# Kernel optimization log

Measured on AMD Instinct MI355X. Metric: run time of the kernel, lower is better.

The kernel has to match this reference:

```python
import jax, jax.numpy as jnp
import numpy as np

B, N, D, H = 2, 2048, 1024, 8
DH = D // H  # head dim = 128


def setup_inputs() -> dict:
    key = jax.random.key(0)
    k0, k1, k2 = jax.random.split(key, 3)
    s = 1.0 / np.sqrt(D).astype(np.float32)
    return {
        "x": jax.random.normal(k0, (B, N, D), dtype=jnp.float32),
        "w_qkv": jax.random.normal(k1, (3 * D, D), dtype=jnp.float32) * s,
        "b_qkv": jnp.zeros((3 * D,), dtype=jnp.float32),
        "w_o": jax.random.normal(k2, (D, D), dtype=jnp.float32) * s,
        "b_o": jnp.zeros((D,), dtype=jnp.float32),
    }


def reference(x, w_qkv, b_qkv, w_o, b_o):
    b, n, d = x.shape
    h = H
    dh = d // h
    # qkv projection (torch Linear: x @ W.T + b)
    qkv = x @ w_qkv.T + b_qkv                      # [b, n, 3d]
    # rearrange 'b n (k d h) -> k b h n d': head index is INNERMOST
    qkv = qkv.reshape(b, n, 3, dh, h)              # [b, n, k, dh, h]
    qkv = jnp.transpose(qkv, (2, 0, 4, 1, 3))      # [k, b, h, n, dh]
    q, k, v = qkv[0], qkv[1], qkv[2]
    # unnormalized attention: NO softmax between the two einsums
    attn = jnp.einsum('bhik,bhjk->bhij', q, k)     # [b, h, n, n]
    out = jnp.einsum('bhik,bhkj->bhij', attn, v)   # [b, h, n, dh]
    # rearrange 'b h n d -> b n (h d)'
    out = jnp.transpose(out, (0, 2, 1, 3)).reshape(b, n, d)
    return out @ w_o.T + b_o
```

## Files before the change

### kernel.cpp

```cpp
#include <hip/hip_runtime.h>
#include <hip/hip_bf16.h>
#include <stdint.h>


typedef __bf16 bf16_t;
typedef __bf16 bf16x4 __attribute__((ext_vector_type(4)));
typedef __bf16 bf16x8 __attribute__((ext_vector_type(8)));
typedef float  fx4    __attribute__((ext_vector_type(4)));
typedef unsigned short u16;
typedef u16 u16x4 __attribute__((ext_vector_type(4)));
typedef u16 u16x8 __attribute__((ext_vector_type(8)));

typedef const void __attribute__((address_space(1)))* gas_ptr;
typedef void __attribute__((address_space(3)))*       las_ptr;

__device__ __forceinline__ void gl_lds16(const void* g, void* l) {
  __builtin_amdgcn_global_load_lds((gas_ptr)g, (las_ptr)l, 16, 0, 0);
}

#define SLAB 262144

__global__ __launch_bounds__(256) void beacon_kernel(float* out, float val, int n)
{
  const int i = blockIdx.x * 256 + threadIdx.x;
  if (i < n) out[i] = val;
}

__global__ __launch_bounds__(256) void conv_xw_kernel(
    const float* __restrict__ x, const float* __restrict__ wq,
    bf16_t* __restrict__ xb, bf16_t* __restrict__ wqkvb)
{
  const int i = blockIdx.x * 256 + threadIdx.x;
  const float* src; bf16_t* dst; int off;
  if (i < 1048576) { src = x;  dst = xb;    off = i; }
  else             { src = wq; dst = wqkvb; off = i - 1048576; }
  const float4 v = ((const float4*)src)[off];
  bf16x4 o;
  o[0] = (bf16_t)v.x; o[1] = (bf16_t)v.y; o[2] = (bf16_t)v.z; o[3] = (bf16_t)v.w;
  ((bf16x4*)dst)[off] = o;
}

__global__ __launch_bounds__(256) void conv_wo_kernel(
    const float* __restrict__ wo, bf16_t* __restrict__ wob)
{
  const int i = blockIdx.x * 256 + threadIdx.x;
  const float4 v = ((const float4*)wo)[i];
  bf16x4 o;
  o[0] = (bf16_t)v.x; o[1] = (bf16_t)v.y; o[2] = (bf16_t)v.z; o[3] = (bf16_t)v.w;
  ((bf16x4*)wob)[i] = o;
}

__global__ __launch_bounds__(256) void mfma_gemm_kernel(
    const bf16_t* __restrict__ A, const bf16_t* __restrict__ Bt,
    const float* __restrict__ bias, bf16_t* __restrict__ outb,
    float* __restrict__ outf, int ldc, int mode)
{
  __shared__ __align__(16) short As[128*32];
  __shared__ __align__(16) short Bs[128*32];
  const int t    = threadIdx.x;
  const int lane = t & 63;
  const int w    = t >> 6;
  const int wr   = (w >> 1) << 6;
  const int wc   = (w & 1) << 6;
  const int lrow = lane & 15;
  const int kq   = (lane >> 4) << 3;
  const int row0 = blockIdx.y * 128;
  const int col0 = blockIdx.x * 128;

  const int i0 = t, i1 = t + 256;
  const bf16_t* a0 = A  + (size_t)(row0 + (i0 >> 2)) * 1024 + ((i0 & 3) << 3);
  const bf16_t* a1 = A  + (size_t)(row0 + (i1 >> 2)) * 1024 + ((i1 & 3) << 3);
  const bf16_t* b0 = Bt + (size_t)(col0 + (i0 >> 2)) * 1024 + ((i0 & 3) << 3);
  const bf16_t* b1 = Bt + (size_t)(col0 + (i1 >> 2)) * 1024 + ((i1 & 3) << 3);
  short* sa0 = &As[i0 * 8]; short* sa1 = &As[i1 * 8];
  short* sb0 = &Bs[i0 * 8]; short* sb1 = &Bs[i1 * 8];

  fx4 acc[4][4] = {};

  for (int k0 = 0; k0 < 1024; k0 += 32) {
    gl_lds16(a0 + k0, sa0);
    gl_lds16(a1 + k0, sa1);
    gl_lds16(b0 + k0, sb0);
    gl_lds16(b1 + k0, sb1);
    __syncthreads();
    bf16x8 af[4], bfr[4];
#pragma unroll
    for (int i = 0; i < 4; ++i)
      af[i] = *(const bf16x8*)&As[(wr + i*16 + lrow)*32 + kq];
#pragma unroll
    for (int j = 0; j < 4; ++j)
      bfr[j] = *(const bf16x8*)&Bs[(wc + j*16 + lrow)*32 + kq];
#pragma unroll
    for (int i = 0; i < 4; ++i)
#pragma unroll
      for (int j = 0; j < 4; ++j)
        acc[i][j] = __builtin_amdgcn_mfma_f32_16x16x32_bf16(af[i], bfr[j], acc[i][j], 0, 0, 0);
    __syncthreads();
  }

#pragma unroll
  for (int j = 0; j < 4; ++j) {
    const int col = col0 + wc + j*16 + lrow;
    const float bv = bias[col];
#pragma unroll
    for (int i = 0; i < 4; ++i) {
#pragma unroll
      for (int r = 0; r < 4; ++r) {
        const int row = row0 + wr + i*16 + ((lane >> 4) << 2) + r;
        const float v = acc[i][j][r] + bv;
        if (mode == 0) outb[(size_t)row * ldc + col] = (bf16_t)v;
        else           outf[(size_t)row * ldc + col] = v;
      }
    }
  }
}

__global__ __launch_bounds__(256) void deint_kernel(
    const bf16_t* __restrict__ qkv, bf16_t* __restrict__ Qb,
    bf16_t* __restrict__ Kb, bf16_t* __restrict__ Vb)
{
  __shared__ u16 L[8][16][132];
  const int t    = threadIdx.x;
  const int kk   = blockIdx.x;
  const int tile = blockIdx.y;
  const int gr0  = tile * 16;
  const u16* src_base = (const u16*)qkv + (size_t)gr0 * 3072 + kk * 1024;

#pragma unroll
  for (int p = 0; p < 2; ++p) {
    const int task = t + p * 256;
    const int r = task >> 5, g = task & 31;
    const u16x8* s = (const u16x8*)(src_base + (size_t)r * 3072 + 32 * g);
    const u16x8 u0 = s[0], u1 = s[1], u2 = s[2], u3 = s[3];
#pragma unroll
    for (int hh = 0; hh < 8; ++hh) {
      u16x4 wv = { u0[hh], u1[hh], u2[hh], u3[hh] };
      *(u16x4*)&L[hh][r][4 * g] = wv;
    }
  }
  __syncthreads();

  const int b  = gr0 >> 11;
  const int n0 = gr0 & 2047;
  bf16_t* base = (kk == 0) ? Qb : (kk == 1 ? Kb : Vb);
#pragma unroll
  for (int p = 0; p < 8; ++p) {
    const int task = t + p * 256;
    const int hh = task >> 8, rem = task & 255;
    const int r = rem >> 4, q = rem & 15;
    const u16x4 w0 = *(const u16x4*)&L[hh][r][8 * q];
    const u16x4 w1 = *(const u16x4*)&L[hh][r][8 * q + 4];
    u16x8 wv = { w0[0], w0[1], w0[2], w0[3], w1[0], w1[1], w1[2], w1[3] };
    *(u16x8*)(base + (size_t)(b * 8 + hh) * SLAB + (size_t)(n0 + r) * 128 + 8 * q) = wv;
  }
}

__global__ __launch_bounds__(256) void kv_part(
    const bf16_t* __restrict__ Kb, const bf16_t* __restrict__ Vb,
    float* __restrict__ Mpart)
{
  __shared__ float Ksf[64][128];
  __shared__ float Vsf[64][64];
  const int t = threadIdx.x;
  const int ch = blockIdx.x >> 1, dh = blockIdx.x & 1, bh = blockIdx.y;
  const bf16_t* Kg = Kb + (size_t)bh * SLAB;
  const bf16_t* Vg = Vb + (size_t)bh * SLAB + dh * 64;
  const int e0 = (t >> 4) * 8, d0 = (t & 15) * 4;
  float acc[8][4] = {};

  for (int sub = 0; sub < 2; ++sub) {
    const int n0 = ch * 128 + sub * 64;
#pragma unroll
    for (int p = 0; p < 4; ++p) {
      const int idx = t + p * 256;
      const int r = idx >> 4, c = (idx & 15) * 8;
      const bf16x8 k8 = *(const bf16x8*)(Kg + (size_t)(n0 + r) * 128 + c);
      float4 f0 = { (float)k8[0], (float)k8[1], (float)k8[2], (float)k8[3] };
      float4 f1 = { (float)k8[4], (float)k8[5], (float)k8[6], (float)k8[7] };
      *(float4*)&Ksf[r][c]     = f0;
      *(float4*)&Ksf[r][c + 4] = f1;
    }
#pragma unroll
    for (int p = 0; p < 2; ++p) {
      const int idx = t + p * 256;
      const int r = idx >> 3, c = (idx & 7) * 8;
      const bf16x8 v8 = *(const bf16x8*)(Vg + (size_t)(n0 + r) * 128 + c);
      float4 f0 = { (float)v8[0], (float)v8[1], (float)v8[2], (float)v8[3] };
      float4 f1 = { (float)v8[4], (float)v8[5], (float)v8[6], (float)v8[7] };
      *(float4*)&Vsf[r][c]     = f0;
      *(float4*)&Vsf[r][c + 4] = f1;
    }
    __syncthreads();
    for (int n = 0; n < 64; ++n) {
      const float4 ka = *(const float4*)&Ksf[n][e0];
      const float4 kb = *(const float4*)&Ksf[n][e0 + 4];
      const float4 vv = *(const float4*)&Vsf[n][d0];
      const float kf[8] = { ka.x, ka.y, ka.z, ka.w, kb.x, kb.y, kb.z, kb.w };
      const float vf[4] = { vv.x, vv.y, vv.z, vv.w };
#pragma unroll
      for (int i = 0; i < 8; ++i)
#pragma unroll
        for (int j = 0; j < 4; ++j) acc[i][j] += kf[i] * vf[j];
    }
    __syncthreads();
  }

  float* op = Mpart + ((size_t)(bh * 16 + ch) << 14) + dh * 64;
#pragma unroll
  for (int i = 0; i < 8; ++i)
    *(float4*)&op[(e0 + i) * 128 + d0] = *(const float4*)&acc[i][0];
}

__global__ __launch_bounds__(256) void reduce_mt(
    const float* __restrict__ Mpart, bf16_t* __restrict__ Mt)
{
  const int t = threadIdx.x, bh = blockIdx.y;
  const int task = blockIdx.x * 256 + t;
  const int eo = task >> 7, d = task & 127;
  const float* base = Mpart + ((size_t)(bh * 16) << 14) + d;
  float s[8] = {};
#pragma unroll
  for (int ch = 0; ch < 16; ++ch) {
    const float* p = base + ((size_t)ch << 14) + (eo * 8) * 128;
#pragma unroll
    for (int j = 0; j < 8; ++j) s[j] += p[j * 128];
  }
  u16x8 wv;
#pragma unroll
  for (int j = 0; j < 8; ++j) { bf16_t b = (bf16_t)s[j]; wv[j] = *(u16*)&b; }
  *(u16x8*)(Mt + (size_t)bh * 16384 + (size_t)d * 128 + eo * 8) = wv;
}

__global__ __launch_bounds__(256) void qm_mfma_kernel(
    const bf16_t* __restrict__ Qb, const bf16_t* __restrict__ Mt,
    bf16_t* __restrict__ O)
{
  __shared__ __align__(16) short As[128*32];
  __shared__ __align__(16) short Bs[128*32];
  const int t    = threadIdx.x;
  const int lane = t & 63;
  const int w    = t >> 6;
  const int wr   = (w >> 1) << 6;
  const int wc   = (w & 1) << 6;
  const int lrow = lane & 15;
  const int kq   = (lane >> 4) << 3;
  const int row0 = blockIdx.x * 128;
  const int bh   = blockIdx.y;
  const bf16_t* A  = Qb + (size_t)bh * SLAB;
  const bf16_t* Bt = Mt + (size_t)bh * 16384;

  const int i0 = t, i1 = t + 256;
  const bf16_t* a0 = A  + (size_t)(row0 + (i0 >> 2)) * 128 + ((i0 & 3) << 3);
  const bf16_t* a1 = A  + (size_t)(row0 + (i1 >> 2)) * 128 + ((i1 & 3) << 3);
  const bf16_t* b0 = Bt + (size_t)(i0 >> 2) * 128 + ((i0 & 3) << 3);
  const bf16_t* b1 = Bt + (size_t)(i1 >> 2) * 128 + ((i1 & 3) << 3);
  short* sa0 = &As[i0 * 8]; short* sa1 = &As[i1 * 8];
  short* sb0 = &Bs[i0 * 8]; short* sb1 = &Bs[i1 * 8];

  fx4 acc[4][4] = {};

  for (int k0 = 0; k0 < 128; k0 += 32) {
    gl_lds16(a0 + k0, sa0);
    gl_lds16(a1 + k0, sa1);
    gl_lds16(b0 + k0, sb0);
    gl_lds16(b1 + k0, sb1);
    __syncthreads();
    bf16x8 af[4], bfr[4];
#pragma unroll
    for (int i = 0; i < 4; ++i)
      af[i] = *(const bf16x8*)&As[(wr + i*16 + lrow)*32 + kq];
#pragma unroll
    for (int j = 0; j < 4; ++j)
      bfr[j] = *(const bf16x8*)&Bs[(wc + j*16 + lrow)*32 + kq];
#pragma unroll
    for (int i = 0; i < 4; ++i)
#pragma unroll
      for (int j = 0; j < 4; ++j)
        acc[i][j] = __builtin_amdgcn_mfma_f32_16x16x32_bf16(af[i], bfr[j], acc[i][j], 0, 0, 0);
    __syncthreads();
  }

  const int b = bh >> 3, h = bh & 7;
  bf16_t* obase = O + (size_t)(b * 2048) * 1024 + h * 128;
#pragma unroll
  for (int j = 0; j < 4; ++j) {
    const int col = wc + j*16 + lrow;
#pragma unroll
    for (int i = 0; i < 4; ++i) {
#pragma unroll
      for (int r = 0; r < 4; ++r) {
        const int row = row0 + wr + i*16 + ((lane >> 4) << 2) + r;
        obase[(size_t)row * 1024 + col] = (bf16_t)acc[i][j][r];
      }
    }
  }
}

extern "C" void kernel_launch(void* const* d_in, const int* in_sizes, int n_in,
                              void* d_out, int out_size, void* d_ws, size_t ws_size,
                              hipStream_t stream) {
  float* out = (float*)d_out;
  dim3 blk(256);

  int ix = -1, iwq = -1, ibq = -1, iwo = -1, ibo = -1;
  if (n_in == 5) {
    for (int i = 0; i < 5; ++i) {
      switch (in_sizes[i]) {
        case 4194304: ix  = i; break;
        case 3145728: iwq = i; break;
        case 3072:    ibq = i; break;
        case 1048576: iwo = i; break;
        case 1024:    ibo = i; break;
        default: break;
      }
    }
  }
  if (ix < 0 || iwq < 0 || ibq < 0 || iwo < 0 || ibo < 0) {
    beacon_kernel<<<dim3((out_size + 255) / 256), blk, 0, stream>>>(out, 50000.0f, out_size);
    return;
  }
  const size_t NEEDED = (size_t)40 * 1048576;
  if (ws_size < NEEDED) {
    beacon_kernel<<<dim3((out_size + 255) / 256), blk, 0, stream>>>(out, 30000.0f, out_size);
    return;
  }

  char* ws = (char*)d_ws;
  bf16_t* xb     = (bf16_t*)(ws);
  bf16_t* Qb     = (bf16_t*)(ws);
  bf16_t* wqkvb  = (bf16_t*)(ws + (size_t)8  * 1048576);
  bf16_t* O      = (bf16_t*)(ws + (size_t)8  * 1048576);
  bf16_t* qkv_rm = (bf16_t*)(ws + (size_t)16 * 1048576);
  float*  Mpart  = (float*) (ws + (size_t)16 * 1048576);
  bf16_t* Mt     = (bf16_t*)(ws + (size_t)32 * 1048576);
  bf16_t* wob    = (bf16_t*)(ws + (size_t)33 * 1048576);
  bf16_t* Kb     = (bf16_t*)d_out;
  bf16_t* Vb     = (bf16_t*)d_out + 16 * SLAB;

  const float* bq = (const float*)d_in[ibq];
  const float* bo = (const float*)d_in[ibo];

  conv_xw_kernel  <<<dim3(7168),    blk, 0, stream>>>((const float*)d_in[ix],
                                                      (const float*)d_in[iwq], xb, wqkvb);
  mfma_gemm_kernel<<<dim3(24, 32),  blk, 0, stream>>>(xb, wqkvb, bq, qkv_rm, out, 3072, 0);
  deint_kernel    <<<dim3(3, 256),  blk, 0, stream>>>(qkv_rm, Qb, Kb, Vb);
  conv_wo_kernel  <<<dim3(1024),    blk, 0, stream>>>((const float*)d_in[iwo], wob);
  kv_part         <<<dim3(32, 16),  blk, 0, stream>>>(Kb, Vb, Mpart);
  reduce_mt       <<<dim3(8, 16),   blk, 0, stream>>>(Mpart, Mt);
  qm_mfma_kernel  <<<dim3(16, 16),  blk, 0, stream>>>(Qb, Mt, O);
  mfma_gemm_kernel<<<dim3(8, 32),   blk, 0, stream>>>(O, wob, bo, qkv_rm, out, 1024, 1);
}
```

Measured before the change: 188.2 us.

## Fold K^T V into output projection weights and permute QKV weights to drop deinterleave

```diff
diff --git a/kernel.cpp b/kernel.cpp
--- a/kernel.cpp
+++ b/kernel.cpp
@@ -8,7 +8,6 @@
 typedef __bf16 bf16x8 __attribute__((ext_vector_type(8)));
 typedef float  fx4    __attribute__((ext_vector_type(4)));
 typedef unsigned short u16;
-typedef u16 u16x4 __attribute__((ext_vector_type(4)));
 typedef u16 u16x8 __attribute__((ext_vector_type(8)));
 
 typedef const void __attribute__((address_space(1)))* gas_ptr;
@@ -18,42 +17,57 @@
   __builtin_amdgcn_global_load_lds((gas_ptr)g, (las_ptr)l, 16, 0, 0);
 }
 
-#define SLAB 262144
-
 __global__ __launch_bounds__(256) void beacon_kernel(float* out, float val, int n)
 {
   const int i = blockIdx.x * 256 + threadIdx.x;
   if (i < n) out[i] = val;
 }
 
-__global__ __launch_bounds__(256) void conv_xw_kernel(
+__global__ __launch_bounds__(256) void conv_all_kernel(
     const float* __restrict__ x, const float* __restrict__ wq,
-    bf16_t* __restrict__ xb, bf16_t* __restrict__ wqkvb)
+    const float* __restrict__ wo, const float* __restrict__ bq,
+    bf16_t* __restrict__ xb, bf16_t* __restrict__ wqkvb,
+    bf16_t* __restrict__ wob, float* __restrict__ bqp)
 {
   const int i = blockIdx.x * 256 + threadIdx.x;
-  const float* src; bf16_t* dst; int off;
-  if (i < 1048576) { src = x;  dst = xb;    off = i; }
-  else             { src = wq; dst = wqkvb; off = i - 1048576; }
-  const float4 v = ((const float4*)src)[off];
-  bf16x4 o;
-  o[0] = (bf16_t)v.x; o[1] = (bf16_t)v.y; o[2] = (bf16_t)v.z; o[3] = (bf16_t)v.w;
-  ((bf16x4*)dst)[off] = o;
-}
-
-__global__ __launch_bounds__(256) void conv_wo_kernel(
-    const float* __restrict__ wo, bf16_t* __restrict__ wob)
-{
-  const int i = blockIdx.x * 256 + threadIdx.x;
-  const float4 v = ((const float4*)wo)[i];
-  bf16x4 o;
-  o[0] = (bf16_t)v.x; o[1] = (bf16_t)v.y; o[2] = (bf16_t)v.z; o[3] = (bf16_t)v.w;
-  ((bf16x4*)wob)[i] = o;
+  if (i < 2097152) {
+    const float* src; bf16_t* dst; int soff, doff;
+    if (i < 1048576) { src = x; dst = xb; soff = i; doff = i; }
+    else if (i < 1835008) {
+      const int j  = i - 1048576;
+      const int rp = j >> 8, g = j & 255;
+      const int kk = rp >> 10, rem = rp & 1023;
+      const int hh = rem >> 7,  dd = rem & 127;
+      const int r  = kk * 1024 + dd * 8 + hh;
+      src = wq; dst = wqkvb; soff = r * 256 + g; doff = j;
+    } else {
+      const int j = i - 1835008;
+      src = wo; dst = wob; soff = j; doff = j;
+    }
+    const float4 v = ((const float4*)src)[soff];
+    bf16x4 o;
+    o[0] = (bf16_t)v.x; o[1] = (bf16_t)v.y; o[2] = (bf16_t)v.z; o[3] = (bf16_t)v.w;
+    ((bf16x4*)dst)[doff] = o;
+  } else if (i < 2097920) {
+    const int j = i - 2097152;
+    float4 v;
+    float* pv = (float*)&v;
+#pragma unroll
+    for (int q = 0; q < 4; ++q) {
+      const int cp = j * 4 + q;
+      const int kk = cp >> 10, rem = cp & 1023;
+      const int hh = rem >> 7,  dd = rem & 127;
+      pv[q] = bq[kk * 1024 + dd * 8 + hh];
+    }
+    ((float4*)bqp)[j] = v;
+  }
 }
 
 __global__ __launch_bounds__(256) void mfma_gemm_kernel(
-    const bf16_t* __restrict__ A, const bf16_t* __restrict__ Bt,
-    const float* __restrict__ bias, bf16_t* __restrict__ outb,
-    float* __restrict__ outf, int ldc, int mode)
+    const bf16_t* __restrict__ A, int lda,
+    const bf16_t* __restrict__ Bt0, int ldb, size_t bt_bstride,
+    const float* __restrict__ bias,
+    bf16_t* __restrict__ outb, float* __restrict__ outf, int ldc, int mode)
 {
   __shared__ __align__(16) short As[128*32];
   __shared__ __align__(16) short Bs[128*32];
@@ -66,12 +80,13 @@
   const int kq   = (lane >> 4) << 3;
   const int row0 = blockIdx.y * 128;
   const int col0 = blockIdx.x * 128;
+  const bf16_t* Bt = Bt0 + (row0 >= 2048 ? bt_bstride : (size_t)0);
 
   const int i0 = t, i1 = t + 256;
-  const bf16_t* a0 = A  + (size_t)(row0 + (i0 >> 2)) * 1024 + ((i0 & 3) << 3);
-  const bf16_t* a1 = A  + (size_t)(row0 + (i1 >> 2)) * 1024 + ((i1 & 3) << 3);
-  const bf16_t* b0 = Bt + (size_t)(col0 + (i0 >> 2)) * 1024 + ((i0 & 3) << 3);
-  const bf16_t* b1 = Bt + (size_t)(col0 + (i1 >> 2)) * 1024 + ((i1 & 3) << 3);
+  const bf16_t* a0 = A  + (size_t)(row0 + (i0 >> 2)) * lda + ((i0 & 3) << 3);
+  const bf16_t* a1 = A  + (size_t)(row0 + (i1 >> 2)) * lda + ((i1 & 3) << 3);
+  const bf16_t* b0 = Bt + (size_t)(col0 + (i0 >> 2)) * ldb + ((i0 & 3) << 3);
+  const bf16_t* b1 = Bt + (size_t)(col0 + (i1 >> 2)) * ldb + ((i1 & 3) << 3);
   short* sa0 = &As[i0 * 8]; short* sa1 = &As[i1 * 8];
   short* sb0 = &Bs[i0 * 8]; short* sb1 = &Bs[i1 * 8];
 
@@ -115,56 +130,16 @@
   }
 }
 
-__global__ __launch_bounds__(256) void deint_kernel(
-    const bf16_t* __restrict__ qkv, bf16_t* __restrict__ Qb,
-    bf16_t* __restrict__ Kb, bf16_t* __restrict__ Vb)
-{
-  __shared__ u16 L[8][16][132];
-  const int t    = threadIdx.x;
-  const int kk   = blockIdx.x;
-  const int tile = blockIdx.y;
-  const int gr0  = tile * 16;
-  const u16* src_base = (const u16*)qkv + (size_t)gr0 * 3072 + kk * 1024;
-
-#pragma unroll
-  for (int p = 0; p < 2; ++p) {
-    const int task = t + p * 256;
-    const int r = task >> 5, g = task & 31;
-    const u16x8* s = (const u16x8*)(src_base + (size_t)r * 3072 + 32 * g);
-    const u16x8 u0 = s[0], u1 = s[1], u2 = s[2], u3 = s[3];
-#pragma unroll
-    for (int hh = 0; hh < 8; ++hh) {
-      u16x4 wv = { u0[hh], u1[hh], u2[hh], u3[hh] };
-      *(u16x4*)&L[hh][r][4 * g] = wv;
-    }
-  }
-  __syncthreads();
-
-  const int b  = gr0 >> 11;
-  const int n0 = gr0 & 2047;
-  bf16_t* base = (kk == 0) ? Qb : (kk == 1 ? Kb : Vb);
-#pragma unroll
-  for (int p = 0; p < 8; ++p) {
-    const int task = t + p * 256;
-    const int hh = task >> 8, rem = task & 255;
-    const int r = rem >> 4, q = rem & 15;
-    const u16x4 w0 = *(const u16x4*)&L[hh][r][8 * q];
-    const u16x4 w1 = *(const u16x4*)&L[hh][r][8 * q + 4];
-    u16x8 wv = { w0[0], w0[1], w0[2], w0[3], w1[0], w1[1], w1[2], w1[3] };
-    *(u16x8*)(base + (size_t)(b * 8 + hh) * SLAB + (size_t)(n0 + r) * 128 + 8 * q) = wv;
-  }
-}
-
 __global__ __launch_bounds__(256) void kv_part(
-    const bf16_t* __restrict__ Kb, const bf16_t* __restrict__ Vb,
-    float* __restrict__ Mpart)
+    const bf16_t* __restrict__ qkv, float* __restrict__ Mpart)
 {
   __shared__ float Ksf[64][128];
   __shared__ float Vsf[64][64];
   const int t = threadIdx.x;
   const int ch = blockIdx.x >> 1, dh = blockIdx.x & 1, bh = blockIdx.y;
-  const bf16_t* Kg = Kb + (size_t)bh * SLAB;
-  const bf16_t* Vg = Vb + (size_t)bh * SLAB + dh * 64;
+  const int b = bh >> 3, h = bh & 7;
+  const bf16_t* Kg = qkv + (size_t)(b * 2048) * 3072 + 1024 + h * 128;
+  const bf16_t* Vg = qkv + (size_t)(b * 2048) * 3072 + 2048 + h * 128 + dh * 64;
   const int e0 = (t >> 4) * 8, d0 = (t & 15) * 4;
   float acc[8][4] = {};
 
@@ -174,7 +149,7 @@
     for (int p = 0; p < 4; ++p) {
       const int idx = t + p * 256;
       const int r = idx >> 4, c = (idx & 15) * 8;
-      const bf16x8 k8 = *(const bf16x8*)(Kg + (size_t)(n0 + r) * 128 + c);
+      const bf16x8 k8 = *(const bf16x8*)(Kg + (size_t)(n0 + r) * 3072 + c);
       float4 f0 = { (float)k8[0], (float)k8[1], (float)k8[2], (float)k8[3] };
       float4 f1 = { (float)k8[4], (float)k8[5], (float)k8[6], (float)k8[7] };
       *(float4*)&Ksf[r][c]     = f0;
@@ -184,7 +159,7 @@
     for (int p = 0; p < 2; ++p) {
       const int idx = t + p * 256;
       const int r = idx >> 3, c = (idx & 7) * 8;
-      const bf16x8 v8 = *(const bf16x8*)(Vg + (size_t)(n0 + r) * 128 + c);
+      const bf16x8 v8 = *(const bf16x8*)(Vg + (size_t)(n0 + r) * 3072 + c);
       float4 f0 = { (float)v8[0], (float)v8[1], (float)v8[2], (float)v8[3] };
       float4 f1 = { (float)v8[4], (float)v8[5], (float)v8[6], (float)v8[7] };
       *(float4*)&Vsf[r][c]     = f0;
@@ -211,29 +186,31 @@
     *(float4*)&op[(e0 + i) * 128 + d0] = *(const float4*)&acc[i][0];
 }
 
-__global__ __launch_bounds__(256) void reduce_mt(
-    const float* __restrict__ Mpart, bf16_t* __restrict__ Mt)
+__global__ __launch_bounds__(256) void reduce_m(
+    const float* __restrict__ Mpart, bf16_t* __restrict__ Mb)
 {
   const int t = threadIdx.x, bh = blockIdx.y;
   const int task = blockIdx.x * 256 + t;
-  const int eo = task >> 7, d = task & 127;
-  const float* base = Mpart + ((size_t)(bh * 16) << 14) + d;
+  const int e = task >> 4, doct = task & 15;
+  const float* base = Mpart + ((size_t)(bh * 16) << 14) + e * 128 + doct * 8;
   float s[8] = {};
 #pragma unroll
   for (int ch = 0; ch < 16; ++ch) {
-    const float* p = base + ((size_t)ch << 14) + (eo * 8) * 128;
-#pragma unroll
-    for (int j = 0; j < 8; ++j) s[j] += p[j * 128];
+    const float* p = base + ((size_t)ch << 14);
+    const float4 v0 = *(const float4*)p;
+    const float4 v1 = *(const float4*)(p + 4);
+    s[0] += v0.x; s[1] += v0.y; s[2] += v0.z; s[3] += v0.w;
+    s[4] += v1.x; s[5] += v1.y; s[6] += v1.z; s[7] += v1.w;
   }
   u16x8 wv;
 #pragma unroll
-  for (int j = 0; j < 8; ++j) { bf16_t b = (bf16_t)s[j]; wv[j] = *(u16*)&b; }
-  *(u16x8*)(Mt + (size_t)bh * 16384 + (size_t)d * 128 + eo * 8) = wv;
-}
-
-__global__ __launch_bounds__(256) void qm_mfma_kernel(
-    const bf16_t* __restrict__ Qb, const bf16_t* __restrict__ Mt,
-    bf16_t* __restrict__ O)
+  for (int j = 0; j < 8; ++j) { bf16_t bb = (bf16_t)s[j]; wv[j] = *(u16*)&bb; }
+  *(u16x8*)(Mb + (size_t)bh * 16384 + e * 128 + doct * 8) = wv;
+}
+
+__global__ __launch_bounds__(256) void wprime_kernel(
+    const bf16_t* __restrict__ wob, const bf16_t* __restrict__ Mb,
+    bf16_t* __restrict__ Wt)
 {
   __shared__ __align__(16) short As[128*32];
   __shared__ __align__(16) short Bs[128*32];
@@ -244,16 +221,16 @@
   const int wc   = (w & 1) << 6;
   const int lrow = lane & 15;
   const int kq   = (lane >> 4) << 3;
-  const int row0 = blockIdx.x * 128;
-  const int bh   = blockIdx.y;
-  const bf16_t* A  = Qb + (size_t)bh * SLAB;
-  const bf16_t* Bt = Mt + (size_t)bh * 16384;
+  const int o0   = blockIdx.x * 128;
+  const int bh   = blockIdx.y, b = bh >> 3, h = bh & 7;
+  const bf16_t* A  = wob + (size_t)o0 * 1024 + h * 128;
+  const bf16_t* Bt = Mb + (size_t)bh * 16384;
 
   const int i0 = t, i1 = t + 256;
-  const bf16_t* a0 = A  + (size_t)(row0 + (i0 >> 2)) * 128 + ((i0 & 3) << 3);
-  const bf16_t* a1 = A  + (size_t)(row0 + (i1 >> 2)) * 128 + ((i1 & 3) << 3);
-  const bf16_t* b0 = Bt + (size_t)(i0 >> 2) * 128 + ((i0 & 3) << 3);
-  const bf16_t* b1 = Bt + (size_t)(i1 >> 2) * 128 + ((i1 & 3) << 3);
+  const bf16_t* a0 = A  + (size_t)(i0 >> 2) * 1024 + ((i0 & 3) << 3);
+  const bf16_t* a1 = A  + (size_t)(i1 >> 2) * 1024 + ((i1 & 3) << 3);
+  const bf16_t* b0 = Bt + (size_t)(i0 >> 2) * 128  + ((i0 & 3) << 3);
+  const bf16_t* b1 = Bt + (size_t)(i1 >> 2) * 128  + ((i1 & 3) << 3);
   short* sa0 = &As[i0 * 8]; short* sa1 = &As[i1 * 8];
   short* sb0 = &Bs[i0 * 8]; short* sb1 = &Bs[i1 * 8];
 
@@ -280,8 +257,7 @@
     __syncthreads();
   }
 
-  const int b = bh >> 3, h = bh & 7;
-  bf16_t* obase = O + (size_t)(b * 2048) * 1024 + h * 128;
+  bf16_t* obase = Wt + (size_t)b * 1048576 + h * 128;
 #pragma unroll
   for (int j = 0; j < 4; ++j) {
     const int col = wc + j*16 + lrow;
@@ -289,7 +265,7 @@
     for (int i = 0; i < 4; ++i) {
 #pragma unroll
       for (int r = 0; r < 4; ++r) {
-        const int row = row0 + wr + i*16 + ((lane >> 4) << 2) + r;
+        const int row = o0 + wr + i*16 + ((lane >> 4) << 2) + r;
         obase[(size_t)row * 1024 + col] = (bf16_t)acc[i][j][r];
       }
     }
@@ -327,26 +303,26 @@
 
   char* ws = (char*)d_ws;
   bf16_t* xb     = (bf16_t*)(ws);
-  bf16_t* Qb     = (bf16_t*)(ws);
   bf16_t* wqkvb  = (bf16_t*)(ws + (size_t)8  * 1048576);
-  bf16_t* O      = (bf16_t*)(ws + (size_t)8  * 1048576);
-  bf16_t* qkv_rm = (bf16_t*)(ws + (size_t)16 * 1048576);
-  float*  Mpart  = (float*) (ws + (size_t)16 * 1048576);
-  bf16_t* Mt     = (bf16_t*)(ws + (size_t)32 * 1048576);
-  bf16_t* wob    = (bf16_t*)(ws + (size_t)33 * 1048576);
-  bf16_t* Kb     = (bf16_t*)d_out;
-  bf16_t* Vb     = (bf16_t*)d_out + 16 * SLAB;
-
-  const float* bq = (const float*)d_in[ibq];
+  bf16_t* wob    = (bf16_t*)(ws + (size_t)14 * 1048576);
+  bf16_t* qkv    = (bf16_t*)(ws + (size_t)16 * 1048576);
+  bf16_t* Mb     = (bf16_t*)(ws);
+  bf16_t* Wt     = (bf16_t*)(ws + (size_t)1  * 1048576);
+  float*  bqp    = (float*)d_out;
+  float*  Mpart  = (float*)d_out;
+
   const float* bo = (const float*)d_in[ibo];
 
-  conv_xw_kernel  <<<dim3(7168),    blk, 0, stream>>>((const float*)d_in[ix],
-                                                      (const float*)d_in[iwq], xb, wqkvb);
-  mfma_gemm_kernel<<<dim3(24, 32),  blk, 0, stream>>>(xb, wqkvb, bq, qkv_rm, out, 3072, 0);
-  deint_kernel    <<<dim3(3, 256),  blk, 0, stream>>>(qkv_rm, Qb, Kb, Vb);
-  conv_wo_kernel  <<<dim3(1024),    blk, 0, stream>>>((const float*)d_in[iwo], wob);
-  kv_part         <<<dim3(32, 16),  blk, 0, stream>>>(Kb, Vb, Mpart);
-  reduce_mt       <<<dim3(8, 16),   blk, 0, stream>>>(Mpart, Mt);
-  qm_mfma_kernel  <<<dim3(16, 16),  blk, 0, stream>>>(Qb, Mt, O);
-  mfma_gemm_kernel<<<dim3(8, 32),   blk, 0, stream>>>(O, wob, bo, qkv_rm, out, 1024, 1);
-}
+  conv_all_kernel <<<dim3(8195),   blk, 0, stream>>>((const float*)d_in[ix],
+                                                     (const float*)d_in[iwq],
+                                                     (const float*)d_in[iwo],
+                                                     (const float*)d_in[ibq],
+                                                     xb, wqkvb, wob, bqp);
+  mfma_gemm_kernel<<<dim3(24, 32), blk, 0, stream>>>(xb, 1024, wqkvb, 1024, 0,
+                                                     bqp, qkv, nullptr, 3072, 0);
+  kv_part         <<<dim3(32, 16), blk, 0, stream>>>(qkv, Mpart);
+  reduce_m        <<<dim3(8, 16),  blk, 0, stream>>>(Mpart, Mb);
+  wprime_kernel   <<<dim3(8, 16),  blk, 0, stream>>>(wob, Mb, Wt);
+  mfma_gemm_kernel<<<dim3(8, 32),  blk, 0, stream>>>(qkv, 3072, Wt, 1024, 1048576,
+                                                     bo, nullptr, out, 1024, 1);
+}
```

Measured after the change: 176.6 us. 1.07x faster.
